# Kernel optimization log

Hardware: AMD Instinct MI355X
Metric: run time of the kernel (lower is better)

Reference implementation:

```python
import jax, jax.numpy as jnp
import numpy as np

D_MODEL = 1024
N_HEADS = 16
N_KV = 8
GROUP = N_HEADS // N_KV  # 2
D_HEAD = D_MODEL // N_HEADS  # 64
SCALE = D_HEAD ** -0.5


def setup_inputs() -> dict:
    key = jax.random.key(0)
    ks = jax.random.split(key, 5)
    s = 0.02
    return {
        "x": jax.random.normal(ks[0], (2, 2048, D_MODEL), dtype=jnp.float32),
        "Wq": jax.random.normal(ks[1], (D_MODEL, D_MODEL), dtype=jnp.float32) * s,
        "Wk": jax.random.normal(ks[2], (N_KV * D_HEAD, D_MODEL), dtype=jnp.float32) * s,
        "Wv": jax.random.normal(ks[3], (N_KV * D_HEAD, D_MODEL), dtype=jnp.float32) * s,
        "Wproj": jax.random.normal(ks[4], (D_MODEL, D_MODEL), dtype=jnp.float32) * s,
    }


def reference(x, Wq, Wk, Wv, Wproj):
    b, t, c = x.shape
    # projections (torch Linear: x @ W.T)
    q = (x @ Wq.T).reshape(b, t, N_KV, GROUP, D_HEAD)  # heads ordered (kv, group)
    k = (x @ Wk.T).reshape(b, t, N_KV, D_HEAD)
    v = (x @ Wv.T).reshape(b, t, N_KV, D_HEAD)
    # repeat_interleave(K/V, group, dim=heads) == broadcast over the group axis,
    # since q head index h maps to kv head h // GROUP.
    scores = jnp.einsum('btkgd,bskd->bkgts', q, k) * SCALE  # (b, kv, g, t, s)
    attn = jax.nn.softmax(scores, axis=-1)
    y = jnp.einsum('bkgts,bskd->btkgd', attn, v)  # (b, t, kv, g, d)
    y = y.reshape(b, t, c)
    return y @ Wproj.T
```

## Files before the change

### kernel.cpp

```cpp
#include <hip/hip_runtime.h>


#define SEQ    2048
#define CDIM   1024
#define KVDIM  512
#define SCL2E  0.18033688011112042f

typedef __attribute__((ext_vector_type(8))) short   bf16x8;
typedef __attribute__((ext_vector_type(4))) float   f32x4;
typedef unsigned short ushort_t;

__device__ __forceinline__ ushort_t f2bf(float f) {
    unsigned u = __float_as_uint(f);
    u += 0x7FFFu + ((u >> 16) & 1u);
    return (ushort_t)(u >> 16);
}
__device__ __forceinline__ float bf2f(ushort_t h) {
    return __uint_as_float(((unsigned)h) << 16);
}
__device__ __forceinline__ void load_lds16(const void* g, void* l) {
    __builtin_amdgcn_global_load_lds(
        (const __attribute__((address_space(1))) void*)g,
        (__attribute__((address_space(3))) void*)l, 16, 0, 0);
}

__global__ __launch_bounds__(256) void cvt_bf16(
    const float* __restrict__ x,  const float* __restrict__ wq,
    const float* __restrict__ wk, const float* __restrict__ wv,
    const float* __restrict__ wp,
    ushort_t* __restrict__ xh,  ushort_t* __restrict__ wqh,
    ushort_t* __restrict__ wkh, ushort_t* __restrict__ wvh,
    ushort_t* __restrict__ wph)
{
    const int i = blockIdx.x * 256 + threadIdx.x;
    const float* src; ushort_t* dst; int off;
    if (i < 1048576)      { src = x;  dst = xh;  off = i; }
    else if (i < 1310720) { src = wq; dst = wqh; off = i - 1048576; }
    else if (i < 1441792) { src = wk; dst = wkh; off = i - 1310720; }
    else if (i < 1572864) { src = wv; dst = wvh; off = i - 1441792; }
    else                  { src = wp; dst = wph; off = i - 1572864; }
    const float4 v = ((const float4*)src)[off];
    ushort4 h;
    h.x = f2bf(v.x); h.y = f2bf(v.y); h.z = f2bf(v.z); h.w = f2bf(v.w);
    ((ushort4*)dst)[off] = h;
}

__global__ __launch_bounds__(256, 4) void gemm64(
    const ushort_t* __restrict__ A, int K,
    const ushort_t* __restrict__ B1, void* __restrict__ C1, int N1, int epi1, float sc1,
    const ushort_t* __restrict__ B2, void* __restrict__ C2, int N2, int epi2, float sc2,
    const ushort_t* __restrict__ B3, void* __restrict__ C3, int N3, int epi3, float sc3)
{
    __shared__ ushort_t sA[128 * 64];
    __shared__ ushort_t sB[64 * 64];

    const int tid = threadIdx.x, wv = tid >> 6, lane = tid & 63;
    const int lm = lane & 15, quad = lane >> 4;

    const int gdx = gridDim.x;
    const int nwg = gdx * gridDim.y;
    int id = blockIdx.y * gdx + blockIdx.x;
    id = (id & 7) * (nwg >> 3) + (id >> 3);
    const int bx = id % gdx;
    const int m0 = (id / gdx) * 128;

    const int t1 = N1 >> 6, t2 = N2 >> 6;
    const ushort_t* B; void* Cv; int n0, Nout, epi; float sc;
    if (bx < t1)           { B = B1; Cv = C1; Nout = N1; epi = epi1; sc = sc1; n0 = bx * 64; }
    else if (bx < t1 + t2) { B = B2; Cv = C2; Nout = N2; epi = epi2; sc = sc2; n0 = (bx - t1) * 64; }
    else                   { B = B3; Cv = C3; Nout = N3; epi = epi3; sc = sc3; n0 = (bx - t1 - t2) * 64; }

    const int mh = wv >> 1, nh = wv & 1;
    const int srow = lane >> 3;
    const int scol = ((lane & 7) ^ ((lane >> 3) & 7)) * 8;

    f32x4 acc[4][2] = {};

    for (int k0 = 0; k0 < K; k0 += 64) {
        __syncthreads();
        #pragma unroll
        for (int i = 0; i < 6; ++i) {
            const int g = wv * 6 + i;
            if (g < 16)
                load_lds16(A + (size_t)(m0 + g * 8 + srow) * K + k0 + scol, sA + g * 512);
            else
                load_lds16(B + (size_t)(n0 + (g - 16) * 8 + srow) * K + k0 + scol, sB + (g - 16) * 512);
        }
        __syncthreads();

        #pragma unroll
        for (int ks = 0; ks < 2; ++ks) {
            const int co = ((ks * 4 + quad) ^ (lm & 7)) * 8;
            bf16x8 a[4], b[2];
            #pragma unroll
            for (int mt = 0; mt < 4; ++mt)
                a[mt] = *(const bf16x8*)&sA[(mh * 64 + mt * 16 + lm) * 64 + co];
            #pragma unroll
            for (int nt = 0; nt < 2; ++nt)
                b[nt] = *(const bf16x8*)&sB[(nh * 32 + nt * 16 + lm) * 64 + co];
            #pragma unroll
            for (int mt = 0; mt < 4; ++mt)
                #pragma unroll
                for (int nt = 0; nt < 2; ++nt)
                    acc[mt][nt] = __builtin_amdgcn_mfma_f32_16x16x32_bf16(a[mt], b[nt], acc[mt][nt], 0, 0, 0);
        }
    }

    if (epi == 0) {
        float* C = (float*)Cv;
        #pragma unroll
        for (int mt = 0; mt < 4; ++mt)
            #pragma unroll
            for (int nt = 0; nt < 2; ++nt)
                #pragma unroll
                for (int r = 0; r < 4; ++r)
                    C[(size_t)(m0 + mh * 64 + mt * 16 + quad * 4 + r) * Nout + n0 + nh * 32 + nt * 16 + lm]
                        = acc[mt][nt][r];
    } else if (epi == 2) {
        ushort_t* C = (ushort_t*)Cv;
        const int bB   = m0 >> 11;
        const int tloc = (m0 & 2047) + mh * 64 + quad * 4;
        #pragma unroll
        for (int mt = 0; mt < 4; ++mt)
            #pragma unroll
            for (int nt = 0; nt < 2; ++nt) {
                const int n = n0 + nh * 32 + nt * 16 + lm;
                ushort4 u;
                u.x = f2bf(acc[mt][nt][0]);
                u.y = f2bf(acc[mt][nt][1]);
                u.z = f2bf(acc[mt][nt][2]);
                u.w = f2bf(acc[mt][nt][3]);
                *(ushort4*)&C[(size_t)(bB * KVDIM + n) * SEQ + tloc + mt * 16] = u;
            }
    } else {
        ushort_t* C = (ushort_t*)Cv;
        #pragma unroll
        for (int mt = 0; mt < 4; ++mt)
            #pragma unroll
            for (int nt = 0; nt < 2; ++nt)
                #pragma unroll
                for (int r = 0; r < 4; ++r)
                    C[(size_t)(m0 + mh * 64 + mt * 16 + quad * 4 + r) * Nout + n0 + nh * 32 + nt * 16 + lm]
                        = f2bf(acc[mt][nt][r] * sc);
    }
}

__global__ __launch_bounds__(256, 2) void attn4(
    const ushort_t* __restrict__ Qh, const ushort_t* __restrict__ Kh,
    const ushort_t* __restrict__ Vth, ushort_t* __restrict__ Yh)
{
    __shared__ ushort_t sK[2][128 * 64];
    __shared__ ushort_t sV[2][64 * 128];

    const int tid = threadIdx.x, wv = tid >> 6, lane = tid & 63;
    const int lm = lane & 15, quad = lane >> 4;
    const int b = blockIdx.y >> 4, h = blockIdx.y & 15, kvh = h >> 1;
    const int t0 = blockIdx.x * 128, tq0 = t0 + wv * 32;

    bf16x8 qh[2][2];
    #pragma unroll
    for (int qg = 0; qg < 2; ++qg) {
        const size_t rb = (size_t)(b * SEQ + tq0 + qg * 16 + lm) * CDIM + h * 64;
        #pragma unroll
        for (int ks = 0; ks < 2; ++ks)
            qh[qg][ks] = *(const bf16x8*)(Qh + rb + ks * 32 + quad * 8);
    }

    const ushort_t* gK = Kh  + (size_t)b * SEQ * KVDIM + kvh * 64;
    const ushort_t* gV = Vth + (size_t)(b * 8 + kvh) * 64 * SEQ;

    const int g0 = (wv & 1) * 8;

    const int srow = lane >> 3;
    const int scol = ((lane & 7) ^ ((lane >> 3) & 7)) * 8;

    int krow[8];
    #pragma unroll
    for (int it = 0; it < 8; ++it) {
        const int lr = (g0 + it) * 8 + srow;
        krow[it] = (lr & 0x60) | ((lr & 0x10) >> 2) | ((lr & 0x0C) << 1) | (lr & 3);
    }

    const int vrow = lane >> 4;
    const int vpos = lane & 15;

    float l_a[2] = {0.0f, 0.0f}, l_b[2] = {0.0f, 0.0f};
    f32x4 O[2][4] = {};

    if (wv < 2) {
        #pragma unroll
        for (int it = 0; it < 8; ++it)
            load_lds16(gK + (size_t)krow[it] * KVDIM + scol,
                       &sK[0][(g0 + it) * 512]);
    } else {
        #pragma unroll
        for (int it = 0; it < 8; ++it) {
            const int d = (g0 + it) * 4 + vrow;
            load_lds16(gV + (size_t)d * SEQ + (vpos ^ (d & 7)) * 8,
                       &sV[0][(g0 + it) * 512]);
        }
    }

    typedef union { bf16x8 v; unsigned u[4]; } pku;

    for (int kt = 0; kt < SEQ / 128; ++kt) {
        const int cur = kt & 1;
        __syncthreads();

        if (kt + 1 < SEQ / 128) {
            const int s1 = (kt + 1) * 128;
            if (wv < 2) {
                #pragma unroll
                for (int it = 0; it < 8; ++it)
                    load_lds16(gK + (size_t)(s1 + krow[it]) * KVDIM + scol,
                               &sK[cur ^ 1][(g0 + it) * 512]);
            } else {
                #pragma unroll
                for (int it = 0; it < 8; ++it) {
                    const int d = (g0 + it) * 4 + vrow;
                    load_lds16(gV + (size_t)d * SEQ + s1 + (vpos ^ (d & 7)) * 8,
                               &sV[cur ^ 1][(g0 + it) * 512]);
                }
            }
        }

        f32x4 st[2][8] = {};
        __builtin_amdgcn_s_setprio(1);
        #pragma unroll
        for (int sti = 0; sti < 8; ++sti)
            #pragma unroll
            for (int ks = 0; ks < 2; ++ks) {
                const int off = (sti * 16 + lm) * 64 + (((ks * 4 + quad) ^ (lm & 7)) * 8);
                const bf16x8 kf = *(const bf16x8*)&sK[cur][off];
                #pragma unroll
                for (int qg = 0; qg < 2; ++qg)
                    st[qg][sti] = __builtin_amdgcn_mfma_f32_16x16x32_bf16(kf, qh[qg][ks], st[qg][sti], 0, 0, 0);
            }
        __builtin_amdgcn_s_setprio(0);

        pku pa[2][4];
        #pragma unroll
        for (int qg = 0; qg < 2; ++qg)
            #pragma unroll
            for (int sti = 0; sti < 8; ++sti) {
                const float p0 = __builtin_amdgcn_exp2f(st[qg][sti][0]);
                const float p1 = __builtin_amdgcn_exp2f(st[qg][sti][1]);
                const float p2 = __builtin_amdgcn_exp2f(st[qg][sti][2]);
                const float p3 = __builtin_amdgcn_exp2f(st[qg][sti][3]);
                if (sti & 1) l_b[qg] += (p0 + p1) + (p2 + p3);
                else         l_a[qg] += (p0 + p1) + (p2 + p3);
                pa[qg][sti >> 1].u[(sti & 1) * 2 + 0] =
                    __builtin_amdgcn_perm(__float_as_uint(p1), __float_as_uint(p0), 0x07060302u);
                pa[qg][sti >> 1].u[(sti & 1) * 2 + 1] =
                    __builtin_amdgcn_perm(__float_as_uint(p3), __float_as_uint(p2), 0x07060302u);
            }

        __builtin_amdgcn_s_setprio(1);
        #pragma unroll
        for (int ks = 0; ks < 4; ++ks) {
            const int co = ((ks * 4 + quad) ^ (lm & 7)) * 8;
            #pragma unroll
            for (int dt = 0; dt < 4; ++dt) {
                const bf16x8 vt = *(const bf16x8*)&sV[cur][(dt * 16 + lm) * 128 + co];
                #pragma unroll
                for (int qg = 0; qg < 2; ++qg)
                    O[qg][dt] = __builtin_amdgcn_mfma_f32_16x16x32_bf16(pa[qg][ks].v, vt, O[qg][dt], 0, 0, 0);
            }
        }
        __builtin_amdgcn_s_setprio(0);
    }

    float l_r[2];
    #pragma unroll
    for (int qg = 0; qg < 2; ++qg) {
        l_r[qg] = l_a[qg] + l_b[qg];
        l_r[qg] += __shfl_xor(l_r[qg], 16);
        l_r[qg] += __shfl_xor(l_r[qg], 32);
    }
    #pragma unroll
    for (int qg = 0; qg < 2; ++qg)
        #pragma unroll
        for (int r = 0; r < 4; ++r) {
            const float lq = __shfl(l_r[qg], (lane & 48) | (quad * 4 + r));
            const float inv = 1.0f / lq;
            const int t = tq0 + qg * 16 + quad * 4 + r;
            const size_t rowb = (size_t)(b * SEQ + t) * CDIM + h * 64;
            #pragma unroll
            for (int dt = 0; dt < 4; ++dt)
                Yh[rowb + dt * 16 + lm] = f2bf(O[qg][dt][r] * inv);
        }
}

extern "C" void kernel_launch(void* const* d_in, const int* in_sizes, int n_in,
                              void* d_out, int out_size, void* d_ws, size_t ws_size,
                              hipStream_t stream)
{
    const float* x     = (const float*)d_in[0];
    const float* Wq    = (const float*)d_in[1];
    const float* Wk    = (const float*)d_in[2];
    const float* Wv    = (const float*)d_in[3];
    const float* Wproj = (const float*)d_in[4];
    float* out = (float*)d_out;

    const int M = 2 * SEQ;

    char* p = (char*)d_ws;
    ushort_t* xh   = (ushort_t*)p; p += (size_t)M * CDIM * 2;
    ushort_t* wqh  = (ushort_t*)p; p += (size_t)CDIM * CDIM * 2;
    ushort_t* wkh  = (ushort_t*)p; p += (size_t)KVDIM * CDIM * 2;
    ushort_t* wvh  = (ushort_t*)p; p += (size_t)KVDIM * CDIM * 2;
    ushort_t* wph  = (ushort_t*)p; p += (size_t)CDIM * CDIM * 2;
    ushort_t* qh   = (ushort_t*)p; p += (size_t)M * CDIM * 2;
    ushort_t* kh   = (ushort_t*)p; p += (size_t)M * KVDIM * 2;
    ushort_t* vth  = (ushort_t*)p; p += (size_t)M * KVDIM * 2;
    ushort_t* yh = xh;

    dim3 blk(256);

    cvt_bf16<<<dim3(7168), blk, 0, stream>>>(
        x, Wq, Wk, Wv, Wproj, xh, wqh, wkh, wvh, wph);

    gemm64<<<dim3(32, 32), blk, 0, stream>>>(
        xh, CDIM,
        wqh, qh,  CDIM,  3, SCL2E,
        wkh, kh,  KVDIM, 3, 1.0f,
        wvh, vth, KVDIM, 2, 1.0f);

    attn4<<<dim3(SEQ / 128, 32), blk, 0, stream>>>(qh, kh, vth, yh);

    gemm64<<<dim3(16, 32), blk, 0, stream>>>(
        yh, CDIM,
        wph, out, CDIM, 0, 1.0f,
        nullptr, nullptr, 0, 0, 1.0f,
        nullptr, nullptr, 0, 0, 1.0f);
}
```

Before: 160.0 us.

## Restructure attention to two waves of 64 queries with 64-key tiles

The attention kernel now runs 128-thread blocks where each of two waves owns 64 query rows, instead of four waves owning 32 rows each. The K/V tile per iteration shrinks from 128 to 64 keys, halving LDS use. Each K/V fragment read from LDS now feeds four MFMAs instead of two. The cost is more accumulator registers per wave (launch bounds 128,1), twice as many loop iterations and barriers, and fewer waves per block to hide latency.

Measured after the change: 168.2 us. 1.05x slower.

```diff
diff --git a/kernel.cpp b/kernel.cpp
--- a/kernel.cpp
+++ b/kernel.cpp
@@ -145,21 +145,21 @@
     }
 }
 
-__global__ __launch_bounds__(256, 2) void attn4(
+__global__ __launch_bounds__(128, 1) void attn5(
     const ushort_t* __restrict__ Qh, const ushort_t* __restrict__ Kh,
     const ushort_t* __restrict__ Vth, ushort_t* __restrict__ Yh)
 {
-    __shared__ ushort_t sK[2][128 * 64];
-    __shared__ ushort_t sV[2][64 * 128];
+    __shared__ ushort_t sK[2][64 * 64];
+    __shared__ ushort_t sV[2][64 * 64];
 
     const int tid = threadIdx.x, wv = tid >> 6, lane = tid & 63;
     const int lm = lane & 15, quad = lane >> 4;
     const int b = blockIdx.y >> 4, h = blockIdx.y & 15, kvh = h >> 1;
-    const int t0 = blockIdx.x * 128, tq0 = t0 + wv * 32;
-
-    bf16x8 qh[2][2];
+    const int t0 = blockIdx.x * 128, tq0 = t0 + wv * 64;
+
+    bf16x8 qh[4][2];
     #pragma unroll
-    for (int qg = 0; qg < 2; ++qg) {
+    for (int qg = 0; qg < 4; ++qg) {
         const size_t rb = (size_t)(b * SEQ + tq0 + qg * 16 + lm) * CDIM + h * 64;
         #pragma unroll
         for (int ks = 0; ks < 2; ++ks)
@@ -168,8 +168,6 @@
 
     const ushort_t* gK = Kh  + (size_t)b * SEQ * KVDIM + kvh * 64;
     const ushort_t* gV = Vth + (size_t)(b * 8 + kvh) * 64 * SEQ;
-
-    const int g0 = (wv & 1) * 8;
 
     const int srow = lane >> 3;
     const int scol = ((lane & 7) ^ ((lane >> 3) & 7)) * 8;
@@ -177,78 +175,68 @@
     int krow[8];
     #pragma unroll
     for (int it = 0; it < 8; ++it) {
-        const int lr = (g0 + it) * 8 + srow;
-        krow[it] = (lr & 0x60) | ((lr & 0x10) >> 2) | ((lr & 0x0C) << 1) | (lr & 3);
-    }
-
-    const int vrow = lane >> 4;
-    const int vpos = lane & 15;
-
-    float l_a[2] = {0.0f, 0.0f}, l_b[2] = {0.0f, 0.0f};
-    f32x4 O[2][4] = {};
-
-    if (wv < 2) {
+        const int lr = it * 8 + srow;
+        krow[it] = (lr & 0x20) | ((lr & 0x10) >> 2) | ((lr & 0x0C) << 1) | (lr & 3);
+    }
+
+    float l_r[4] = {0.0f, 0.0f, 0.0f, 0.0f};
+    f32x4 O[4][4] = {};
+
+    if (wv == 0) {
         #pragma unroll
         for (int it = 0; it < 8; ++it)
-            load_lds16(gK + (size_t)krow[it] * KVDIM + scol,
-                       &sK[0][(g0 + it) * 512]);
+            load_lds16(gK + (size_t)krow[it] * KVDIM + scol, &sK[0][it * 512]);
     } else {
         #pragma unroll
-        for (int it = 0; it < 8; ++it) {
-            const int d = (g0 + it) * 4 + vrow;
-            load_lds16(gV + (size_t)d * SEQ + (vpos ^ (d & 7)) * 8,
-                       &sV[0][(g0 + it) * 512]);
-        }
+        for (int it = 0; it < 8; ++it)
+            load_lds16(gV + (size_t)(it * 8 + srow) * SEQ + scol, &sV[0][it * 512]);
     }
 
     typedef union { bf16x8 v; unsigned u[4]; } pku;
 
-    for (int kt = 0; kt < SEQ / 128; ++kt) {
+    for (int kt = 0; kt < SEQ / 64; ++kt) {
         const int cur = kt & 1;
         __syncthreads();
 
-        if (kt + 1 < SEQ / 128) {
-            const int s1 = (kt + 1) * 128;
-            if (wv < 2) {
+        if (kt + 1 < SEQ / 64) {
+            const int s1 = (kt + 1) * 64;
+            if (wv == 0) {
                 #pragma unroll
                 for (int it = 0; it < 8; ++it)
                     load_lds16(gK + (size_t)(s1 + krow[it]) * KVDIM + scol,
-                               &sK[cur ^ 1][(g0 + it) * 512]);
+                               &sK[cur ^ 1][it * 512]);
             } else {
                 #pragma unroll
-                for (int it = 0; it < 8; ++it) {
-                    const int d = (g0 + it) * 4 + vrow;
-                    load_lds16(gV + (size_t)d * SEQ + s1 + (vpos ^ (d & 7)) * 8,
-                               &sV[cur ^ 1][(g0 + it) * 512]);
-                }
-            }
-        }
-
-        f32x4 st[2][8] = {};
+                for (int it = 0; it < 8; ++it)
+                    load_lds16(gV + (size_t)(it * 8 + srow) * SEQ + s1 + scol,
+                               &sV[cur ^ 1][it * 512]);
+            }
+        }
+
+        f32x4 st[4][4] = {};
         __builtin_amdgcn_s_setprio(1);
         #pragma unroll
-        for (int sti = 0; sti < 8; ++sti)
+        for (int sti = 0; sti < 4; ++sti)
             #pragma unroll
             for (int ks = 0; ks < 2; ++ks) {
                 const int off = (sti * 16 + lm) * 64 + (((ks * 4 + quad) ^ (lm & 7)) * 8);
                 const bf16x8 kf = *(const bf16x8*)&sK[cur][off];
                 #pragma unroll
-                for (int qg = 0; qg < 2; ++qg)
+                for (int qg = 0; qg < 4; ++qg)
                     st[qg][sti] = __builtin_amdgcn_mfma_f32_16x16x32_bf16(kf, qh[qg][ks], st[qg][sti], 0, 0, 0);
             }
         __builtin_amdgcn_s_setprio(0);
 
-        pku pa[2][4];
-        #pragma unroll
-        for (int qg = 0; qg < 2; ++qg)
-            #pragma unroll
-            for (int sti = 0; sti < 8; ++sti) {
+        pku pa[4][2];
+        #pragma unroll
+        for (int qg = 0; qg < 4; ++qg)
+            #pragma unroll
+            for (int sti = 0; sti < 4; ++sti) {
                 const float p0 = __builtin_amdgcn_exp2f(st[qg][sti][0]);
                 const float p1 = __builtin_amdgcn_exp2f(st[qg][sti][1]);
                 const float p2 = __builtin_amdgcn_exp2f(st[qg][sti][2]);
                 const float p3 = __builtin_amdgcn_exp2f(st[qg][sti][3]);
-                if (sti & 1) l_b[qg] += (p0 + p1) + (p2 + p3);
-                else         l_a[qg] += (p0 + p1) + (p2 + p3);
+                l_r[qg] += (p0 + p1) + (p2 + p3);
                 pa[qg][sti >> 1].u[(sti & 1) * 2 + 0] =
                     __builtin_amdgcn_perm(__float_as_uint(p1), __float_as_uint(p0), 0x07060302u);
                 pa[qg][sti >> 1].u[(sti & 1) * 2 + 1] =
@@ -257,28 +245,26 @@
 
         __builtin_amdgcn_s_setprio(1);
         #pragma unroll
-        for (int ks = 0; ks < 4; ++ks) {
+        for (int ks = 0; ks < 2; ++ks) {
             const int co = ((ks * 4 + quad) ^ (lm & 7)) * 8;
             #pragma unroll
             for (int dt = 0; dt < 4; ++dt) {
-                const bf16x8 vt = *(const bf16x8*)&sV[cur][(dt * 16 + lm) * 128 + co];
-                #pragma unroll
-                for (int qg = 0; qg < 2; ++qg)
+                const bf16x8 vt = *(const bf16x8*)&sV[cur][(dt * 16 + lm) * 64 + co];
+                #pragma unroll
+                for (int qg = 0; qg < 4; ++qg)
                     O[qg][dt] = __builtin_amdgcn_mfma_f32_16x16x32_bf16(pa[qg][ks].v, vt, O[qg][dt], 0, 0, 0);
             }
         }
         __builtin_amdgcn_s_setprio(0);
     }
 
-    float l_r[2];
     #pragma unroll
-    for (int qg = 0; qg < 2; ++qg) {
-        l_r[qg] = l_a[qg] + l_b[qg];
+    for (int qg = 0; qg < 4; ++qg) {
         l_r[qg] += __shfl_xor(l_r[qg], 16);
         l_r[qg] += __shfl_xor(l_r[qg], 32);
     }
     #pragma unroll
-    for (int qg = 0; qg < 2; ++qg)
+    for (int qg = 0; qg < 4; ++qg)
         #pragma unroll
         for (int r = 0; r < 4; ++r) {
             const float lq = __shfl(l_r[qg], (lane & 48) | (quad * 4 + r));
@@ -326,7 +312,7 @@
         wkh, kh,  KVDIM, 3, 1.0f,
         wvh, vth, KVDIM, 2, 1.0f);
 
-    attn4<<<dim3(SEQ / 128, 32), blk, 0, stream>>>(qh, kh, vth, yh);
+    attn5<<<dim3(SEQ / 128, 32), dim3(128), 0, stream>>>(qh, kh, vth, yh);
 
     gemm64<<<dim3(16, 32), blk, 0, stream>>>(
         yh, CDIM,
```
